# Optimization experiments

Measured on AMD Instinct MI355X. Metric: run time of the kernel, lower is better.

Reference implementation:

```python
import jax, jax.numpy as jnp
import numpy as np
from jax import lax

B, FREQ, TIME = 32, 256, 4096   # batch, freq bins, time frames
PAD_LEN = 256                   # cfg['n_peaks']
KSIZE = 5                       # cfg['blur_kernel']
SIGMA = 1.0                     # cfg['blur_sigma']


def setup_inputs() -> dict:
    key = jax.random.key(0)
    return {"spec_tensor": jax.random.normal(key, (B, FREQ, TIME), dtype=jnp.float32)}


def _peak_from_features(f):
    # local maxima along time (1x3) and freq (3x1), SAME padding, stride 1
    neg = jnp.asarray(-jnp.inf, f.dtype)
    max_t = lax.reduce_window(f, neg, lax.max, (1, 1, 3), (1, 1, 1), 'SAME')
    max_f = lax.reduce_window(f, neg, lax.max, (1, 3, 1), (1, 1, 1), 'SAME')
    peaks = ((f == max_t) & (f == max_f)).astype(f.dtype)
    mn = jnp.min(f, axis=(1, 2), keepdims=True)
    mx = jnp.max(f, axis=(1, 2), keepdims=True)
    return peaks * ((f - mn) / (mx - mn))


def _gaussian_blur(x):
    # separable gaussian blur with reflect padding (torchvision semantics)
    half = KSIZE // 2
    coords = jnp.arange(KSIZE, dtype=x.dtype) - half
    g = jnp.exp(-0.5 * (coords / SIGMA) ** 2)
    g = g / jnp.sum(g)
    x4 = jnp.pad(x, ((0, 0), (half, half), (half, half)), mode='reflect')[:, None]  # [B,1,F+2h,T+2h]
    kf = g.reshape(1, 1, KSIZE, 1)
    kt = g.reshape(1, 1, 1, KSIZE)
    y = lax.conv_general_dilated(x4, kf, (1, 1), 'VALID')
    y = lax.conv_general_dilated(y, kt, (1, 1), 'VALID')
    return y[:, 0]


def _extract(flat):
    # compact nonzero entries (row-major order) into fixed PAD_LEN slots, zero padded;
    # entries beyond PAD_LEN are truncated (scatter mode='drop').
    mask = flat > 0
    pos = jnp.cumsum(mask.astype(jnp.int32)) - 1
    dest = jnp.where(mask, pos, PAD_LEN)  # out-of-range -> dropped
    idx = jnp.zeros(PAD_LEN, jnp.int32).at[dest].set(
        jnp.arange(flat.shape[0], dtype=jnp.int32), mode='drop')
    val = jnp.zeros(PAD_LEN, flat.dtype).at[dest].set(flat, mode='drop')
    freq = (idx // TIME).astype(flat.dtype) / FREQ
    time = (idx % TIME).astype(flat.dtype) / TIME
    return jnp.stack([freq, time, val], axis=0)  # [3, PAD_LEN]


def reference(spec_tensor):
    p = _peak_from_features(spec_tensor)
    p = _gaussian_blur(p)
    p = _peak_from_features(p)
    return jax.vmap(_extract)(p.reshape(B, FREQ * TIME))  # [B, 3, PAD_LEN]
```

## Files before the change

kernel.cpp:

```cpp
#include <hip/hip_runtime.h>

#define NB 32
#define NF 256
#define NT 4096
#define PAD_LEN 256

#define TF 16
#define TT 128

#define TS 64
#define NSTRIP (NT / TS)

#define G0 0.054488684f
#define G1 0.24420134f
#define G2 0.40261995f

__device__ __forceinline__ float blur5(float a, float b, float c, float d, float e) {
    return G0 * (a + b) + G1 * (c + d) + G2 * e;
}
__device__ __forceinline__ float4 blur5v(const float4& a, const float4& b, const float4& c,
                                         const float4& d, const float4& e) {
    return make_float4(blur5(a.x, b.x, c.x, d.x, e.x), blur5(a.y, b.y, c.y, d.y, e.y),
                       blur5(a.z, b.z, c.z, d.z, e.z), blur5(a.w, b.w, c.w, d.w, e.w));
}

#define SW 140
#define SW4 35
#define RS 24
#define RP 22
#define RV 18

#define R1_WORDS (RS * SW)
#define R2_WORDS (RP * SW)

#define MPAD 20

__device__ __forceinline__ int reflectF(int i) {
    i = (i < 0) ? -i : i;
    return (i >= NF) ? (2 * NF - 2 - i) : i;
}
__device__ __forceinline__ unsigned encf(float x) {
    unsigned u = __float_as_uint(x);
    return (u & 0x80000000u) ? ~u : (u | 0x80000000u);
}
__device__ __forceinline__ float decf(unsigned e) {
    unsigned u = (e & 0x80000000u) ? (e ^ 0x80000000u) : ~e;
    return __uint_as_float(u);
}

#define MM_OFF 0
#define CNT_OFF 1024
#define PFX_OFF (1024 + NB * NF * 32 * 4)

__global__ __launch_bounds__(256) void k_init(float* __restrict__ out, unsigned* __restrict__ mm) {
    int tid = blockIdx.x * 256 + threadIdx.x;
    if (tid < NB * 3 * PAD_LEN) out[tid] = 0.0f;
    if (tid < NB) {
        mm[tid * 4 + 0] = 0xFFFFFFFFu;
        mm[tid * 4 + 1] = 0u;
        mm[tid * 4 + 2] = 0xFFFFFFFFu;
        mm[tid * 4 + 3] = 0u;
    }
}

__global__ __launch_bounds__(256) void k_minmax(const float* __restrict__ spec, unsigned* __restrict__ mm) {
    const int b = blockIdx.y;
    const float4* p = (const float4*)(spec + (size_t)b * NF * NT);
    const int base4 = blockIdx.x * 4096;
    float lmin = __builtin_inff(), lmax = -__builtin_inff();
    for (int i = threadIdx.x; i < 4096; i += 256) {
        float4 v = p[base4 + i];
        lmin = fminf(lmin, fminf(fminf(v.x, v.y), fminf(v.z, v.w)));
        lmax = fmaxf(lmax, fmaxf(fmaxf(v.x, v.y), fmaxf(v.z, v.w)));
    }
    for (int off = 32; off; off >>= 1) {
        lmin = fminf(lmin, __shfl_down(lmin, off));
        lmax = fmaxf(lmax, __shfl_down(lmax, off));
    }
    __shared__ float rmn[4], rmx[4];
    int wave = threadIdx.x >> 6, lane = threadIdx.x & 63;
    if (lane == 0) { rmn[wave] = lmin; rmx[wave] = lmax; }
    __syncthreads();
    if (threadIdx.x == 0) {
        for (int w = 1; w < 4; w++) { lmin = fminf(lmin, rmn[w]); lmax = fmaxf(lmax, rmx[w]); }
        atomicMin(&mm[b * 4 + 0], encf(lmin));
        atomicMax(&mm[b * 4 + 1], encf(lmax));
    }
}


template<int J> __device__ __forceinline__ float getj(const float4& v) {
    if constexpr (J == 0) return v.x;
    else if constexpr (J == 1) return v.y;
    else if constexpr (J == 2) return v.z;
    else return v.w;
}

template<bool DP, bool DH, bool DQ, int J>
__device__ __forceinline__ void march_step(
    const float4& r0, const float4& r1, const float4& r2, const float4& r3,
    float4& Sa, float4& Sb, float4& Sc,
    float4& V0, float4& V1, float4& V2, float4& V3, float4& V4,
    float4& Bm, float4& Bc, float4& Bp,
    int& c0, int& c1, int& c2, int& c3,
    float& lmin, float& lmax,
    const int lane, const int sid, const float mn, const float rinv, const int hb)
{
    const float NEGF = -__builtin_inff();
    float4 X = make_float4(getj<J>(r0), getj<J>(r1), getj<J>(r2), getj<J>(r3));
    Sa = Sb; Sb = Sc; Sc = X;
    if constexpr (DP) {
        float up0 = __shfl_up(Sb.w, 1);
        float dn3 = __shfl_down(Sb.x, 1);
        if (lane == 0)  up0 = NEGF;
        if (lane == 63) dn3 = NEGF;
        float4 P;
        { const float x = Sb.x; const bool pk = (x >= Sa.x) && (x >= Sc.x) && (x >= up0)  && (x >= Sb.y); P.x = pk ? (x - mn) * rinv : 0.0f; }
        { const float x = Sb.y; const bool pk = (x >= Sa.y) && (x >= Sc.y) && (x >= Sb.x) && (x >= Sb.z); P.y = pk ? (x - mn) * rinv : 0.0f; }
        { const float x = Sb.z; const bool pk = (x >= Sa.z) && (x >= Sc.z) && (x >= Sb.y) && (x >= Sb.w); P.z = pk ? (x - mn) * rinv : 0.0f; }
        { const float x = Sb.w; const bool pk = (x >= Sa.w) && (x >= Sc.w) && (x >= Sb.z) && (x >= dn3); P.w = pk ? (x - mn) * rinv : 0.0f; }
        const float pzm = __shfl_up(P.z, 1);
        const float pwm = __shfl_up(P.w, 1);
        const float pxp = __shfl_down(P.x, 1);
        const float pyp = __shfl_down(P.y, 1);
        float4 Vn;
        Vn.x = blur5(pzm, P.z, pwm, P.y, P.x);
        Vn.y = blur5(pwm, P.w, P.x, P.z, P.y);
        Vn.z = blur5(P.x, pxp, P.y, P.w, P.z);
        Vn.w = blur5(P.y, pyp, P.z, pxp, P.w);
        if (lane == 0)  { Vn.x = blur5(P.z, P.z, P.y, P.y, P.x);
                          Vn.y = blur5(P.y, P.w, P.x, P.z, P.y); }
        if (lane == 63) { Vn.z = blur5(P.x, P.z, P.y, P.w, P.z);
                          Vn.w = blur5(P.y, P.y, P.z, P.z, P.w); }
        V0 = V1; V1 = V2; V2 = V3; V3 = V4; V4 = Vn;
    }
    if constexpr (DH) {
        const int h = hb + J;
        float4 Bn;
        if ((unsigned)h < (unsigned)NT) {
            Bn = blur5v(V0, V4, V1, V3, V2);
            if (sid == 0) {
                if (h == 0)      Bn = blur5v(V4, V4, V3, V3, V2);
                else if (h == 1) Bn = blur5v(V2, V4, V1, V3, V2);
            }
            if (sid == NSTRIP - 1) {
                if (h == NT - 2)      Bn = blur5v(V0, V2, V1, V3, V2);
                else if (h == NT - 1) Bn = blur5v(V0, V0, V1, V1, V2);
            }
        } else {
            Bn = make_float4(NEGF, NEGF, NEGF, NEGF);
        }
        Bm = Bc; Bc = Bp; Bp = Bn;
    }
    if constexpr (DQ) {
        float u0 = __shfl_up(Bc.w, 1);
        float d3 = __shfl_down(Bc.x, 1);
        if (lane == 0)  u0 = NEGF;
        if (lane == 63) d3 = NEGF;
        { const float x = Bc.x; const bool pk = (x >= Bm.x) && (x >= Bp.x) && (x >= u0)   && (x >= Bc.y); c0 += (pk && (x > 0.0f)) ? 1 : 0; }
        { const float x = Bc.y; const bool pk = (x >= Bm.y) && (x >= Bp.y) && (x >= Bc.x) && (x >= Bc.z); c1 += (pk && (x > 0.0f)) ? 1 : 0; }
        { const float x = Bc.z; const bool pk = (x >= Bm.z) && (x >= Bp.z) && (x >= Bc.y) && (x >= Bc.w); c2 += (pk && (x > 0.0f)) ? 1 : 0; }
        { const float x = Bc.w; const bool pk = (x >= Bm.w) && (x >= Bp.w) && (x >= Bc.z) && (x >= d3); c3 += (pk && (x > 0.0f)) ? 1 : 0; }
        lmin = fminf(lmin, fminf(fminf(Bc.x, Bc.y), fminf(Bc.z, Bc.w)));
        lmax = fmaxf(lmax, fmaxf(fmaxf(Bc.x, Bc.y), fmaxf(Bc.z, Bc.w)));
    }
}

__global__ __launch_bounds__(256) void k_march(const float* __restrict__ spec,
                                               unsigned* __restrict__ mm,
                                               int* __restrict__ counts2) {
    const int b = blockIdx.y;
    const int lane = threadIdx.x & 63;
    const int wv = threadIdx.x >> 6;
    const int sid = blockIdx.x * 4 + wv;
    const int T0 = sid * TS;

    const float mn = decf(mm[b * 4 + 0]);
    const float mx = decf(mm[b * 4 + 1]);
    const float rinv = 1.0f / (mx - mn);

    const float NEGF = -__builtin_inff();
    const float4 NEG4 = make_float4(NEGF, NEGF, NEGF, NEGF);

    __shared__ __align__(16) float sStage[4][256 * MPAD];
    float* myS = sStage[wv];

    const int lrow = lane >> 2;
    const int lq = lane & 3;
    const float* gb = spec + (size_t)b * NF * NT;

    float4 R[16];
    float4 A[4];

#define GLOAD(J) do {                                                           \
    const int tg = T0 - 16 + 16 * (J);                                          \
    if ((unsigned)tg < (unsigned)NT) {                                          \
        const float* gp = gb + (size_t)lrow * NT + tg + 4 * lq;                 \
        _Pragma("unroll")                                                       \
        for (int i = 0; i < 16; ++i)                                            \
            R[i] = *(const float4*)(gp + (size_t)(16 * i) * NT);                \
    } else {                                                                    \
        _Pragma("unroll")                                                       \
        for (int i = 0; i < 16; ++i) R[i] = NEG4;                               \
    }                                                                           \
} while (0)

#define SWRITE() do {                                                           \
    _Pragma("unroll")                                                           \
    for (int i = 0; i < 16; ++i) {                                              \
        const int row_ = 16 * i + lrow;                                         \
        const int q_ = (row_ * 5 + lq) ^ ((row_ >> 2) & 7);                     \
        *(float4*)(myS + 4 * q_) = R[i];                                        \
    }                                                                           \
} while (0)

#define SREAD(C) do {                                                           \
    _Pragma("unroll")                                                           \
    for (int j = 0; j < 4; ++j) {                                               \
        const int row_ = 4 * lane + j;                                          \
        const int q_ = (row_ * 5 + ((C) >> 2)) ^ (lane & 7);                    \
        A[j] = *(const float4*)(myS + 4 * q_);                                  \
    }                                                                           \
} while (0)

    float4 Sa = NEG4, Sb = NEG4, Sc = NEG4;
    float4 V0 = NEG4, V1 = NEG4, V2 = NEG4, V3 = NEG4, V4 = NEG4;
    float4 Bm = NEG4, Bc = NEG4, Bp = NEG4;
    int c0 = 0, c1 = 0, c2 = 0, c3 = 0;
    float lmin = __builtin_inff(), lmax = NEGF;

#define MARGS Sa, Sb, Sc, V0, V1, V2, V3, V4, Bm, Bc, Bp, c0, c1, c2, c3, lmin, lmax, lane, sid, mn, rinv

#define SET_FULL(C, HB) do { SREAD(C); const int hb_ = (HB);                    \
    march_step<true, true, true, 0>(A[0], A[1], A[2], A[3], MARGS, hb_);        \
    march_step<true, true, true, 1>(A[0], A[1], A[2], A[3], MARGS, hb_);        \
    march_step<true, true, true, 2>(A[0], A[1], A[2], A[3], MARGS, hb_);        \
    march_step<true, true, true, 3>(A[0], A[1], A[2], A[3], MARGS, hb_); } while (0)

    GLOAD(0);
    SWRITE();
    GLOAD(1);
    SREAD(12);
    march_step<false, false, false, 0>(A[0], A[1], A[2], A[3], MARGS, 0);
    march_step<false, false, false, 1>(A[0], A[1], A[2], A[3], MARGS, 0);
    march_step<true,  false, false, 2>(A[0], A[1], A[2], A[3], MARGS, 0);
    march_step<true,  false, false, 3>(A[0], A[1], A[2], A[3], MARGS, 0);
    SWRITE();
    GLOAD(2);
    {
        const int hb_ = T0 - 3;
        SREAD(0);
        march_step<true, false, false, 0>(A[0], A[1], A[2], A[3], MARGS, hb_);
        march_step<true, false, false, 1>(A[0], A[1], A[2], A[3], MARGS, hb_);
        march_step<true, true,  false, 2>(A[0], A[1], A[2], A[3], MARGS, hb_);
        march_step<true, true,  false, 3>(A[0], A[1], A[2], A[3], MARGS, hb_);
    }
    SET_FULL(4,  T0 + 1);
    SET_FULL(8,  T0 + 5);
    SET_FULL(12, T0 + 9);
    SWRITE(); GLOAD(3);
    SET_FULL(0,  T0 + 13); SET_FULL(4,  T0 + 17); SET_FULL(8,  T0 + 21); SET_FULL(12, T0 + 25);
    SWRITE(); GLOAD(4);
    SET_FULL(0,  T0 + 29); SET_FULL(4,  T0 + 33); SET_FULL(8,  T0 + 37); SET_FULL(12, T0 + 41);
    SWRITE(); GLOAD(5);
    SET_FULL(0,  T0 + 45); SET_FULL(4,  T0 + 49); SET_FULL(8,  T0 + 53); SET_FULL(12, T0 + 57);
    SWRITE();
    SET_FULL(0,  T0 + 61);

#undef SET_FULL
#undef GLOAD
#undef SWRITE
#undef SREAD
#undef MARGS

    int* sc = (int*)&sStage[0][0];
    __syncthreads();
    sc[threadIdx.x * 4 + 0] = c0;
    sc[threadIdx.x * 4 + 1] = c1;
    sc[threadIdx.x * 4 + 2] = c2;
    sc[threadIdx.x * 4 + 3] = c3;
    __syncthreads();
    if ((wv & 1) == 0) {
        const int p = (threadIdx.x + 64) * 4;
        const int cc = sid >> 1;
        const int fr = 4 * lane;
        counts2[(b * NF + fr + 0) * 32 + cc] = c0 + sc[p + 0];
        counts2[(b * NF + fr + 1) * 32 + cc] = c1 + sc[p + 1];
        counts2[(b * NF + fr + 2) * 32 + cc] = c2 + sc[p + 2];
        counts2[(b * NF + fr + 3) * 32 + cc] = c3 + sc[p + 3];
    }

    for (int off = 32; off; off >>= 1) {
        lmin = fminf(lmin, __shfl_down(lmin, off));
        lmax = fmaxf(lmax, __shfl_down(lmax, off));
    }
    if (lane == 0) {
        atomicMin(&mm[b * 4 + 2], encf(lmin));
        atomicMax(&mm[b * 4 + 3], encf(lmax));
    }
}

__device__ __forceinline__ void blur_tile(const float* __restrict__ sb_base,
                                          int f0, int t0, float mn, float rinv,
                                          float* sR1, float* sR2, int tid,
                                          bool f_lo, bool f_hi, bool t_lo, bool t_hi) {
    const float NEG = -__builtin_inff();
    float* sS = sR1;
    float* sV = sR1;
    float* sB = sR2;
    float4* sS4 = (float4*)sR1;
    float4* sP4 = (float4*)sR2;
    float4* sV4 = (float4*)sR1;
    float4* sB4 = (float4*)sR2;

    const bool f_edge = f_lo || f_hi;
    const bool t_edge = t_lo || t_hi;
    const int lane = tid & 63;

    if (!f_edge && !t_edge) {
        const float4* gp = (const float4*)(sb_base + (size_t)(f0 - 4) * NT + (t0 - 4));
        for (int i = tid; i < RS * 34; i += 256) {
            int r = i / 34, c = i - r * 34;
            sS4[r * SW4 + c] = gp[r * (NT / 4) + c];
        }
    } else {
        for (int i = tid; i < RS * 34; i += 256) {
            int r = i / 34, c = i - r * 34;
            int gf = f0 - 4 + r;
            int gc0 = t0 - 4 + 4 * c;
            float4 v = make_float4(NEG, NEG, NEG, NEG);
            if ((unsigned)gf < NF && (unsigned)gc0 < NT)
                v = *(const float4*)(sb_base + (size_t)gf * NT + gc0);
            sS4[r * SW4 + c] = v;
        }
    }
    __syncthreads();

    for (int i = tid; i < RP * 34; i += 256) {
        int r = i / 34, g = i - r * 34;
        const float4 c4 = sS4[(r + 1) * SW4 + g];
        const float4 u4 = sS4[r * SW4 + g];
        const float4 d4 = sS4[(r + 2) * SW4 + g];
        float lm = __shfl_up(c4.w, 1);
        float rp = __shfl_down(c4.x, 1);
        if (lane == 0 && g > 0)   lm = sS[(r + 1) * SW + 4 * g - 1];
        if (lane == 63 && g < 33) rp = sS[(r + 1) * SW + 4 * g + 4];
        float4 o;
        o.x = (c4.x >= lm   && c4.x >= c4.y && c4.x >= u4.x && c4.x >= d4.x) ? (c4.x - mn) * rinv : 0.0f;
        o.y = (c4.y >= c4.x && c4.y >= c4.z && c4.y >= u4.y && c4.y >= d4.y) ? (c4.y - mn) * rinv : 0.0f;
        o.z = (c4.z >= c4.y && c4.z >= c4.w && c4.z >= u4.z && c4.z >= d4.z) ? (c4.z - mn) * rinv : 0.0f;
        o.w = (c4.w >= c4.z && c4.w >= rp   && c4.w >= u4.w && c4.w >= d4.w) ? (c4.w - mn) * rinv : 0.0f;
        if (g == 0) o.x = 0.0f;
        if (g == 33) o.w = 0.0f;
        sP4[r * SW4 + g] = o;
    }
    __syncthreads();

    if (!f_edge) {
        for (int i = tid; i < RV * 34; i += 256) {
            int r = i / 34, g = i - r * 34;
            const float4 p0 = sP4[r * SW4 + g];
            const float4 p1 = sP4[(r + 1) * SW4 + g];
            const float4 p2 = sP4[(r + 2) * SW4 + g];
            const float4 p3 = sP4[(r + 3) * SW4 + g];
            const float4 p4 = sP4[(r + 4) * SW4 + g];
            sV4[r * SW4 + g] = blur5v(p0, p4, p1, p3, p2);
        }
    } else {
        for (int i = tid; i < RV * 34; i += 256) {
            int r = i / 34, g = i - r * 34;
            const int gf = f0 - 1 + r;
            const int r0 = reflectF(gf - 2) - (f0 - 3);
            const int r1 = reflectF(gf - 1) - (f0 - 3);
            const int r2 = gf - (f0 - 3);
            const int r3 = reflectF(gf + 1) - (f0 - 3);
            const int r4 = reflectF(gf + 2) - (f0 - 3);
            const float4 p0 = sP4[r0 * SW4 + g];
            const float4 p1 = sP4[r1 * SW4 + g];
            const float4 p2 = sP4[r2 * SW4 + g];
            const float4 p3 = sP4[r3 * SW4 + g];
            const float4 p4 = sP4[r4 * SW4 + g];
            sV4[r * SW4 + g] = blur5v(p0, p4, p1, p3, p2);
        }
    }
    __syncthreads();

    for (int i = tid; i < RV * 32; i += 256) {
        int r = i >> 5, g = 1 + (i & 31);
        const float4 A = sV4[r * SW4 + g - 1];
        const float4 B = sV4[r * SW4 + g];
        const float4 C = sV4[r * SW4 + g + 1];
        float4 o;
        o.x = blur5(A.z, B.z, A.w, B.y, B.x);
        o.y = blur5(A.w, B.w, B.x, B.z, B.y);
        o.z = blur5(B.x, C.x, B.y, B.w, B.z);
        o.w = blur5(B.y, C.y, B.z, C.x, B.w);
        if (t_lo && g == 1) {
            o.x = blur5(B.z, B.z, B.y, B.y, B.x);
            o.y = blur5(B.y, B.w, B.x, B.z, B.y);
        }
        if (t_hi && g == 32) {
            o.z = blur5(B.x, B.z, B.y, B.w, B.z);
            o.w = blur5(B.y, B.y, B.z, B.z, B.w);
        }
        if ((f_lo && r == 0) || (f_hi && r == 17)) o = make_float4(NEG, NEG, NEG, NEG);
        sB4[r * SW4 + g] = o;
    }
    for (int i = tid; i < RV * 2; i += 256) {
        int r = i >> 1;
        int hi = i & 1;
        int s = hi ? 132 : 3;
        const float* vr = sV + r * SW;
        float v = blur5(vr[s - 2], vr[s + 2], vr[s - 1], vr[s + 1], vr[s]);
        if ((hi ? t_hi : t_lo) || (f_lo && r == 0) || (f_hi && r == 17)) v = NEG;
        sB[r * SW + s] = v;
    }
    __syncthreads();
}

struct Win8 {
    float c[8], l[8], rr[8], u[8], d[8];
};
__device__ __forceinline__ void load_win8(const float4* sB4, int r, int m, Win8& w) {
    const int g = 1 + 2 * m;
    const float4 Cm = sB4[(r + 1) * SW4 + g - 1];
    const float4 C0 = sB4[(r + 1) * SW4 + g];
    const float4 C1 = sB4[(r + 1) * SW4 + g + 1];
    const float4 C2 = sB4[(r + 1) * SW4 + g + 2];
    const float4 U0 = sB4[r * SW4 + g];
    const float4 U1 = sB4[r * SW4 + g + 1];
    const float4 D0 = sB4[(r + 2) * SW4 + g];
    const float4 D1 = sB4[(r + 2) * SW4 + g + 1];
    w.c[0] = C0.x; w.c[1] = C0.y; w.c[2] = C0.z; w.c[3] = C0.w;
    w.c[4] = C1.x; w.c[5] = C1.y; w.c[6] = C1.z; w.c[7] = C1.w;
    w.l[0] = Cm.w; w.l[1] = C0.x; w.l[2] = C0.y; w.l[3] = C0.z;
    w.l[4] = C0.w; w.l[5] = C1.x; w.l[6] = C1.y; w.l[7] = C1.z;
    w.rr[0] = C0.y; w.rr[1] = C0.z; w.rr[2] = C0.w; w.rr[3] = C1.x;
    w.rr[4] = C1.y; w.rr[5] = C1.z; w.rr[6] = C1.w; w.rr[7] = C2.x;
    w.u[0] = U0.x; w.u[1] = U0.y; w.u[2] = U0.z; w.u[3] = U0.w;
    w.u[4] = U1.x; w.u[5] = U1.y; w.u[6] = U1.z; w.u[7] = U1.w;
    w.d[0] = D0.x; w.d[1] = D0.y; w.d[2] = D0.z; w.d[3] = D0.w;
    w.d[4] = D1.x; w.d[5] = D1.y; w.d[6] = D1.z; w.d[7] = D1.w;
}

__global__ __launch_bounds__(256) void k_prefix(const float* __restrict__ spec,
                                                unsigned* __restrict__ mm,
                                                int* __restrict__ counts2,
                                                int* __restrict__ prefix2) {
    const int b = blockIdx.x;
    const int tid = threadIdx.x;
    const float mn2 = decf(mm[b * 4 + 2]);
    if (mn2 != 0.0f) {
        __shared__ __align__(16) float sR1[R1_WORDS];
        __shared__ __align__(16) float sR2[R2_WORDS];
        const float4* sB4 = (const float4*)sR2;
        const float mn = decf(mm[b * 4 + 0]);
        const float mx = decf(mm[b * 4 + 1]);
        const float rinv = 1.0f / (mx - mn);
        const float* sb_base = spec + (size_t)b * NF * NT;
        int* pcnt = (int*)sR1;
        for (int ty = 0; ty < NF / TF; ++ty)
        for (int tx = 0; tx < NT / TT; ++tx) {
            blur_tile(sb_base, ty * TF, tx * TT, mn, rinv, sR1, sR2, tid,
                      ty == 0, ty == NF / TF - 1, tx == 0, tx == NT / TT - 1);
            const int r = tid & 15, m = tid >> 4;
            Win8 w;
            load_win8(sB4, r, m, w);
            int cnt = 0;
#pragma unroll
            for (int k = 0; k < 8; k++) {
                float x = w.c[k];
                bool pk = (x >= w.l[k]) && (x >= w.rr[k]) && (x >= w.u[k]) && (x >= w.d[k]);
                cnt += (pk && (x > mn2)) ? 1 : 0;
            }
            (void)m;
            const int lane = tid & 63, wvv = tid >> 6;
            int cs = cnt;
            cs += __shfl_down(cs, 32);
            cs += __shfl_down(cs, 16);
            if (lane < 16) pcnt[wvv * 16 + lane] = cs;
            __syncthreads();
            if (tid < 16)
                counts2[(b * NF + ty * TF + tid) * 32 + tx] =
                    pcnt[tid] + pcnt[16 + tid] + pcnt[32 + tid] + pcnt[48 + tid];
            __syncthreads();
        }
    }
    const int* cb = counts2 + b * NF * 32;
    int* pb = prefix2 + b * NF * 32;
    int local[32];
    int s = 0;
    for (int c = 0; c < 32; c++) {
        local[c] = cb[tid * 32 + c];
        s += local[c];
    }
    __shared__ int tot[256];
    tot[tid] = s;
    __syncthreads();
    for (int off = 1; off < 256; off <<= 1) {
        int v = (tid >= off) ? tot[tid - off] : 0;
        __syncthreads();
        tot[tid] += v;
        __syncthreads();
    }
    int run = tot[tid] - s;
    for (int c = 0; c < 32; c++) {
        pb[tid * 32 + c] = run;
        run += local[c];
    }
}

__global__ __launch_bounds__(256) void k_extract(const float* __restrict__ spec, unsigned* __restrict__ mm,
                                                 const int* __restrict__ prefix2, float* __restrict__ out) {
    const int b = blockIdx.z;
    const int f0 = blockIdx.y * TF;
    const int t0 = blockIdx.x * TT;
    const int c0 = blockIdx.x;
    if (prefix2[(b * NF + f0) * 32 + c0] >= PAD_LEN) return;

    const int tid = threadIdx.x;
    __shared__ __align__(16) float sR1[R1_WORDS];
    __shared__ __align__(16) float sR2[R2_WORDS];
    const float4* sB4 = (const float4*)sR2;

    const float mn = decf(mm[b * 4 + 0]);
    const float mx = decf(mm[b * 4 + 1]);
    const float rinv = 1.0f / (mx - mn);
    const float mn2 = decf(mm[b * 4 + 2]);
    const float mx2 = decf(mm[b * 4 + 3]);
    const float rinv2 = 1.0f / (mx2 - mn2);
    const float* sb_base = spec + (size_t)b * NF * NT;

    const bool f_lo = (blockIdx.y == 0), f_hi = (blockIdx.y == NF / TF - 1);
    const bool t_lo = (blockIdx.x == 0), t_hi = (blockIdx.x == NT / TT - 1);
    blur_tile(sb_base, f0, t0, mn, rinv, sR1, sR2, tid, f_lo, f_hi, t_lo, t_hi);

    const int r = tid & 15, m = tid >> 4;
    const int gf = f0 + r;
    const int base = prefix2[(b * NF + gf) * 32 + c0];
    Win8 w;
    load_win8(sB4, r, m, w);
    bool pos[8];
    int mycnt = 0;
#pragma unroll
    for (int k = 0; k < 8; k++) {
        float x = w.c[k];
        pos[k] = (x >= w.l[k]) && (x >= w.rr[k]) && (x >= w.u[k]) && (x >= w.d[k]) && (x > mn2);
        mycnt += pos[k] ? 1 : 0;
    }
    const int lane = tid & 63, wv = tid >> 6, p = (tid >> 4) & 3;
    int s = mycnt;
    int t1 = __shfl_up(s, 16); if (p >= 1) s += t1;
    int t2 = __shfl_up(s, 32); if (p >= 2) s += t2;
    __shared__ int wtot[4][16];
    if (p == 3) wtot[wv][lane & 15] = s;
    __syncthreads();
    int woff = 0;
    for (int w2 = 0; w2 < wv; ++w2) woff += wtot[w2][r];
    int rank = base + woff + (s - mycnt);
#pragma unroll
    for (int k = 0; k < 8; k++) {
        if (pos[k]) {
            if (rank < PAD_LEN) {
                int gc = t0 + 8 * m + k;
                out[b * 768 + rank]       = (float)gf * (1.0f / 256.0f);
                out[b * 768 + 256 + rank] = (float)gc * (1.0f / 4096.0f);
                out[b * 768 + 512 + rank] = (w.c[k] - mn2) * rinv2;
            }
            rank++;
        }
    }
}

extern "C" void kernel_launch(void* const* d_in, const int* in_sizes, int n_in,
                              void* d_out, int out_size, void* d_ws, size_t ws_size,
                              hipStream_t stream) {
    const float* spec = (const float*)d_in[0];
    float* out = (float*)d_out;
    unsigned* mm = (unsigned*)((char*)d_ws + MM_OFF);
    int* counts2 = (int*)((char*)d_ws + CNT_OFF);
    int* prefix2 = (int*)((char*)d_ws + PFX_OFF);

    k_init<<<96, 256, 0, stream>>>(out, mm);
    k_minmax<<<dim3(64, NB), 256, 0, stream>>>(spec, mm);
    k_march<<<dim3(NSTRIP / 4, NB), 256, 0, stream>>>(spec, mm, counts2);
    k_prefix<<<NB, 256, 0, stream>>>(spec, mm, counts2, prefix2);
    dim3 tgrid(NT / TT, NF / TF, NB);
    k_extract<<<tgrid, 256, 0, stream>>>(spec, mm, prefix2, out);
}
```

Baseline: 330.7 us.

## Fuse prefix and extract into one per-batch tail kernel; shrink march smem padding

Merges the prefix-scan kernel and the tiled extract kernel into a single per-batch kernel. It walks tiles in row-major order, skips tiles with zero peaks and stops once the running prefix reaches PAD_LEN. This removes one launch and the large grid of extract blocks, most of which exit early or do redundant blur work. In exchange, extraction runs serially over tiles within one block per batch, which is only 32 blocks. Separately, the march shared-memory stride drops from 5 to 4 float4 per row (MPAD 20→16), and the read swizzle now uses the row-based XOR so it matches the write side.

```diff
diff --git a/kernel.cpp b/kernel.cpp
--- a/kernel.cpp
+++ b/kernel.cpp
@@ -33,7 +33,7 @@
 #define R1_WORDS (RS * SW)
 #define R2_WORDS (RP * SW)
 
-#define MPAD 20
+#define MPAD 16
 
 __device__ __forceinline__ int reflectF(int i) {
     i = (i < 0) ? -i : i;
@@ -209,7 +209,7 @@
     _Pragma("unroll")                                                           \
     for (int i = 0; i < 16; ++i) {                                              \
         const int row_ = 16 * i + lrow;                                         \
-        const int q_ = (row_ * 5 + lq) ^ ((row_ >> 2) & 7);                     \
+        const int q_ = (row_ * 4 + lq) ^ ((row_ >> 2) & 7);                     \
         *(float4*)(myS + 4 * q_) = R[i];                                        \
     }                                                                           \
 } while (0)
@@ -218,7 +218,7 @@
     _Pragma("unroll")                                                           \
     for (int j = 0; j < 4; ++j) {                                               \
         const int row_ = 4 * lane + j;                                          \
-        const int q_ = (row_ * 5 + ((C) >> 2)) ^ (lane & 7);                    \
+        const int q_ = (row_ * 4 + ((C) >> 2)) ^ ((row_ >> 2) & 7);             \
         A[j] = *(const float4*)(myS + 4 * q_);                                  \
     }                                                                           \
 } while (0)
@@ -443,21 +443,26 @@
     w.d[4] = D1.x; w.d[5] = D1.y; w.d[6] = D1.z; w.d[7] = D1.w;
 }
 
-__global__ __launch_bounds__(256) void k_prefix(const float* __restrict__ spec,
-                                                unsigned* __restrict__ mm,
-                                                int* __restrict__ counts2,
-                                                int* __restrict__ prefix2) {
+__global__ __launch_bounds__(256) void k_tail(const float* __restrict__ spec,
+                                              unsigned* __restrict__ mm,
+                                              int* __restrict__ counts2,
+                                              int* __restrict__ prefix2,
+                                              float* __restrict__ out) {
     const int b = blockIdx.x;
     const int tid = threadIdx.x;
+    __shared__ __align__(16) float sR1[R1_WORDS];
+    __shared__ __align__(16) float sR2[R2_WORDS];
+    const float4* sB4 = (const float4*)sR2;
+
+    const float mn = decf(mm[b * 4 + 0]);
+    const float mx = decf(mm[b * 4 + 1]);
+    const float rinv = 1.0f / (mx - mn);
     const float mn2 = decf(mm[b * 4 + 2]);
+    const float mx2 = decf(mm[b * 4 + 3]);
+    const float rinv2 = 1.0f / (mx2 - mn2);
+    const float* sb_base = spec + (size_t)b * NF * NT;
+
     if (mn2 != 0.0f) {
-        __shared__ __align__(16) float sR1[R1_WORDS];
-        __shared__ __align__(16) float sR2[R2_WORDS];
-        const float4* sB4 = (const float4*)sR2;
-        const float mn = decf(mm[b * 4 + 0]);
-        const float mx = decf(mm[b * 4 + 1]);
-        const float rinv = 1.0f / (mx - mn);
-        const float* sb_base = spec + (size_t)b * NF * NT;
         int* pcnt = (int*)sR1;
         for (int ty = 0; ty < NF / TF; ++ty)
         for (int tx = 0; tx < NT / TT; ++tx) {
@@ -486,88 +491,87 @@
             __syncthreads();
         }
     }
+
     const int* cb = counts2 + b * NF * 32;
     int* pb = prefix2 + b * NF * 32;
-    int local[32];
-    int s = 0;
-    for (int c = 0; c < 32; c++) {
-        local[c] = cb[tid * 32 + c];
-        s += local[c];
-    }
-    __shared__ int tot[256];
-    tot[tid] = s;
-    __syncthreads();
-    for (int off = 1; off < 256; off <<= 1) {
-        int v = (tid >= off) ? tot[tid - off] : 0;
+    {
+        int local[32];
+        int s = 0;
+        for (int c = 0; c < 32; c++) {
+            local[c] = cb[tid * 32 + c];
+            s += local[c];
+        }
+        __shared__ int tot[256];
+        tot[tid] = s;
         __syncthreads();
-        tot[tid] += v;
+        for (int off = 1; off < 256; off <<= 1) {
+            int v = (tid >= off) ? tot[tid - off] : 0;
+            __syncthreads();
+            tot[tid] += v;
+            __syncthreads();
+        }
+        int run = tot[tid] - s;
+        for (int c = 0; c < 32; c++) {
+            pb[tid * 32 + c] = run;
+            run += local[c];
+        }
+    }
+
+    __shared__ int sInfo[2];
+    __shared__ int wtot[4][16];
+    for (int t = 0; t < (NF / TF) * (NT / TT); ++t) {
+        const int ty = t >> 5, tx = t & 31;
+        const int f0 = ty * TF, t0 = tx * TT;
         __syncthreads();
-    }
-    int run = tot[tid] - s;
-    for (int c = 0; c < 32; c++) {
-        pb[tid * 32 + c] = run;
-        run += local[c];
-    }
-}
-
-__global__ __launch_bounds__(256) void k_extract(const float* __restrict__ spec, unsigned* __restrict__ mm,
-                                                 const int* __restrict__ prefix2, float* __restrict__ out) {
-    const int b = blockIdx.z;
-    const int f0 = blockIdx.y * TF;
-    const int t0 = blockIdx.x * TT;
-    const int c0 = blockIdx.x;
-    if (prefix2[(b * NF + f0) * 32 + c0] >= PAD_LEN) return;
-
-    const int tid = threadIdx.x;
-    __shared__ __align__(16) float sR1[R1_WORDS];
-    __shared__ __align__(16) float sR2[R2_WORDS];
-    const float4* sB4 = (const float4*)sR2;
-
-    const float mn = decf(mm[b * 4 + 0]);
-    const float mx = decf(mm[b * 4 + 1]);
-    const float rinv = 1.0f / (mx - mn);
-    const float mn2 = decf(mm[b * 4 + 2]);
-    const float mx2 = decf(mm[b * 4 + 3]);
-    const float rinv2 = 1.0f / (mx2 - mn2);
-    const float* sb_base = spec + (size_t)b * NF * NT;
-
-    const bool f_lo = (blockIdx.y == 0), f_hi = (blockIdx.y == NF / TF - 1);
-    const bool t_lo = (blockIdx.x == 0), t_hi = (blockIdx.x == NT / TT - 1);
-    blur_tile(sb_base, f0, t0, mn, rinv, sR1, sR2, tid, f_lo, f_hi, t_lo, t_hi);
-
-    const int r = tid & 15, m = tid >> 4;
-    const int gf = f0 + r;
-    const int base = prefix2[(b * NF + gf) * 32 + c0];
-    Win8 w;
-    load_win8(sB4, r, m, w);
-    bool pos[8];
-    int mycnt = 0;
+        if (tid == 0) sInfo[0] = pb[f0 * 32 + tx];
+        int tc = 0;
+        if (tid < 16) tc = cb[(f0 + tid) * 32 + tx];
+        tc += __shfl_down(tc, 8, 16);
+        tc += __shfl_down(tc, 4, 16);
+        tc += __shfl_down(tc, 2, 16);
+        tc += __shfl_down(tc, 1, 16);
+        if (tid == 0) sInfo[1] = tc;
+        __syncthreads();
+        if (sInfo[0] >= PAD_LEN) break;
+        if (sInfo[1] == 0) continue;
+
+        const bool f_lo = (ty == 0), f_hi = (ty == NF / TF - 1);
+        const bool t_lo = (tx == 0), t_hi = (tx == NT / TT - 1);
+        blur_tile(sb_base, f0, t0, mn, rinv, sR1, sR2, tid, f_lo, f_hi, t_lo, t_hi);
+
+        const int r = tid & 15, m = tid >> 4;
+        const int gf = f0 + r;
+        const int base = pb[gf * 32 + tx];
+        Win8 w;
+        load_win8(sB4, r, m, w);
+        bool pos[8];
+        int mycnt = 0;
 #pragma unroll
-    for (int k = 0; k < 8; k++) {
-        float x = w.c[k];
-        pos[k] = (x >= w.l[k]) && (x >= w.rr[k]) && (x >= w.u[k]) && (x >= w.d[k]) && (x > mn2);
-        mycnt += pos[k] ? 1 : 0;
-    }
-    const int lane = tid & 63, wv = tid >> 6, p = (tid >> 4) & 3;
-    int s = mycnt;
-    int t1 = __shfl_up(s, 16); if (p >= 1) s += t1;
-    int t2 = __shfl_up(s, 32); if (p >= 2) s += t2;
-    __shared__ int wtot[4][16];
-    if (p == 3) wtot[wv][lane & 15] = s;
-    __syncthreads();
-    int woff = 0;
-    for (int w2 = 0; w2 < wv; ++w2) woff += wtot[w2][r];
-    int rank = base + woff + (s - mycnt);
+        for (int k = 0; k < 8; k++) {
+            float x = w.c[k];
+            pos[k] = (x >= w.l[k]) && (x >= w.rr[k]) && (x >= w.u[k]) && (x >= w.d[k]) && (x > mn2);
+            mycnt += pos[k] ? 1 : 0;
+        }
+        const int lane = tid & 63, wv = tid >> 6, p = (tid >> 4) & 3;
+        int s = mycnt;
+        int t1 = __shfl_up(s, 16); if (p >= 1) s += t1;
+        int t2 = __shfl_up(s, 32); if (p >= 2) s += t2;
+        if (p == 3) wtot[wv][lane & 15] = s;
+        __syncthreads();
+        int woff = 0;
+        for (int w2 = 0; w2 < wv; ++w2) woff += wtot[w2][r];
+        int rank = base + woff + (s - mycnt);
 #pragma unroll
-    for (int k = 0; k < 8; k++) {
-        if (pos[k]) {
-            if (rank < PAD_LEN) {
-                int gc = t0 + 8 * m + k;
-                out[b * 768 + rank]       = (float)gf * (1.0f / 256.0f);
-                out[b * 768 + 256 + rank] = (float)gc * (1.0f / 4096.0f);
-                out[b * 768 + 512 + rank] = (w.c[k] - mn2) * rinv2;
+        for (int k = 0; k < 8; k++) {
+            if (pos[k]) {
+                if (rank < PAD_LEN) {
+                    int gc = t0 + 8 * m + k;
+                    out[b * 768 + rank]       = (float)gf * (1.0f / 256.0f);
+                    out[b * 768 + 256 + rank] = (float)gc * (1.0f / 4096.0f);
+                    out[b * 768 + 512 + rank] = (w.c[k] - mn2) * rinv2;
+                }
+                rank++;
             }
-            rank++;
         }
     }
 }
@@ -584,7 +588,5 @@
     k_init<<<96, 256, 0, stream>>>(out, mm);
     k_minmax<<<dim3(64, NB), 256, 0, stream>>>(spec, mm);
     k_march<<<dim3(NSTRIP / 4, NB), 256, 0, stream>>>(spec, mm, counts2);
-    k_prefix<<<NB, 256, 0, stream>>>(spec, mm, counts2, prefix2);
-    dim3 tgrid(NT / TT, NF / TF, NB);
-    k_extract<<<tgrid, 256, 0, stream>>>(spec, mm, prefix2, out);
-}
+    k_tail<<<NB, 256, 0, stream>>>(spec, mm, counts2, prefix2, out);
+}
```

Result: slower. 392.5 us (+18.7%).

## Halve march strip width to 32 frames and raise k_march occupancy

Applied to the files above, without the earlier changes.

Reduces the time strip handled per wavefront from 64 to 32 frames, so each load stage stages 8 float4 rows instead of 16. This shrinks register and LDS footprint and adds a launch bound of 3 blocks per SM. It also changes the LDS swizzle layout, clamps edge loads in place of the conditional -inf fill (with explicit masking at the first and last strips), and sums the per-wave counts across all 4 waves in a block. The cost is a larger halo-to-work ratio, since the 3-frame halo is now recomputed over fewer frames, and twice as many blocks.

```diff
diff --git a/kernel.cpp b/kernel.cpp
--- a/kernel.cpp
+++ b/kernel.cpp
@@ -8,7 +8,7 @@
 #define TF 16
 #define TT 128
 
-#define TS 64
+#define TS 32
 #define NSTRIP (NT / TS)
 
 #define G0 0.054488684f
@@ -32,8 +32,6 @@
 
 #define R1_WORDS (RS * SW)
 #define R2_WORDS (RP * SW)
-
-#define MPAD 20
 
 __device__ __forceinline__ int reflectF(int i) {
     i = (i < 0) ? -i : i;
@@ -166,9 +164,9 @@
     }
 }
 
-__global__ __launch_bounds__(256) void k_march(const float* __restrict__ spec,
-                                               unsigned* __restrict__ mm,
-                                               int* __restrict__ counts2) {
+__global__ __launch_bounds__(256, 3) void k_march(const float* __restrict__ spec,
+                                                  unsigned* __restrict__ mm,
+                                                  int* __restrict__ counts2) {
     const int b = blockIdx.y;
     const int lane = threadIdx.x & 63;
     const int wv = threadIdx.x >> 6;
@@ -182,45 +180,35 @@
     const float NEGF = -__builtin_inff();
     const float4 NEG4 = make_float4(NEGF, NEGF, NEGF, NEGF);
 
-    __shared__ __align__(16) float sStage[4][256 * MPAD];
-    float* myS = sStage[wv];
-
-    const int lrow = lane >> 2;
-    const int lq = lane & 3;
+    __shared__ __align__(16) float sBuf[4][2048];
+    float4* myS4 = (float4*)sBuf[wv];
+
+    const int srow = lane >> 1;
+    const int sq = lane & 1;
     const float* gb = spec + (size_t)b * NF * NT;
 
-    float4 R[16];
+    float4 R[8];
     float4 A[4];
 
-#define GLOAD(J) do {                                                           \
-    const int tg = T0 - 16 + 16 * (J);                                          \
-    if ((unsigned)tg < (unsigned)NT) {                                          \
-        const float* gp = gb + (size_t)lrow * NT + tg + 4 * lq;                 \
-        _Pragma("unroll")                                                       \
-        for (int i = 0; i < 16; ++i)                                            \
-            R[i] = *(const float4*)(gp + (size_t)(16 * i) * NT);                \
-    } else {                                                                    \
-        _Pragma("unroll")                                                       \
-        for (int i = 0; i < 16; ++i) R[i] = NEG4;                               \
-    }                                                                           \
+#define GLOAD(G) do {                                                           \
+    int tg_ = T0 - 8 + 8 * (G) + 4 * sq;                                        \
+    tg_ = (tg_ < 0) ? 0 : ((tg_ > NT - 4) ? (NT - 4) : tg_);                    \
+    const float* gp_ = gb + (size_t)srow * NT + tg_;                            \
+    _Pragma("unroll")                                                           \
+    for (int i = 0; i < 8; ++i)                                                 \
+        R[i] = *(const float4*)(gp_ + (size_t)(32 * i) * NT);                   \
 } while (0)
 
-#define SWRITE() do {                                                           \
+#define WRITE() do {                                                            \
     _Pragma("unroll")                                                           \
-    for (int i = 0; i < 16; ++i) {                                              \
-        const int row_ = 16 * i + lrow;                                         \
-        const int q_ = (row_ * 5 + lq) ^ ((row_ >> 2) & 7);                     \
-        *(float4*)(myS + 4 * q_) = R[i];                                        \
-    }                                                                           \
+    for (int i = 0; i < 8; ++i)                                                 \
+        myS4[(64 * i + lane) ^ ((lane >> 3) & 7)] = R[i];                       \
 } while (0)
 
-#define SREAD(C) do {                                                           \
+#define SREAD(QC) do {                                                          \
     _Pragma("unroll")                                                           \
-    for (int j = 0; j < 4; ++j) {                                               \
-        const int row_ = 4 * lane + j;                                          \
-        const int q_ = (row_ * 5 + ((C) >> 2)) ^ (lane & 7);                    \
-        A[j] = *(const float4*)(myS + 4 * q_);                                  \
-    }                                                                           \
+    for (int j = 0; j < 4; ++j)                                                 \
+        A[j] = myS4[(8 * lane + 2 * j + (QC)) ^ (lane & 7)];                    \
 } while (0)
 
     float4 Sa = NEG4, Sb = NEG4, Sc = NEG4;
@@ -231,22 +219,22 @@
 
 #define MARGS Sa, Sb, Sc, V0, V1, V2, V3, V4, Bm, Bc, Bp, c0, c1, c2, c3, lmin, lmax, lane, sid, mn, rinv
 
-#define SET_FULL(C, HB) do { SREAD(C); const int hb_ = (HB);                    \
+#define SET_FULL(HB) do { const int hb_ = (HB);                                 \
     march_step<true, true, true, 0>(A[0], A[1], A[2], A[3], MARGS, hb_);        \
     march_step<true, true, true, 1>(A[0], A[1], A[2], A[3], MARGS, hb_);        \
     march_step<true, true, true, 2>(A[0], A[1], A[2], A[3], MARGS, hb_);        \
     march_step<true, true, true, 3>(A[0], A[1], A[2], A[3], MARGS, hb_); } while (0)
 
-    GLOAD(0);
-    SWRITE();
-    GLOAD(1);
-    SREAD(12);
+    GLOAD(0); WRITE(); GLOAD(1);
+
+    SREAD(1);
+    if (sid == 0) { A[0] = NEG4; A[1] = NEG4; A[2] = NEG4; A[3] = NEG4; }
     march_step<false, false, false, 0>(A[0], A[1], A[2], A[3], MARGS, 0);
     march_step<false, false, false, 1>(A[0], A[1], A[2], A[3], MARGS, 0);
     march_step<true,  false, false, 2>(A[0], A[1], A[2], A[3], MARGS, 0);
     march_step<true,  false, false, 3>(A[0], A[1], A[2], A[3], MARGS, 0);
-    SWRITE();
-    GLOAD(2);
+
+    WRITE(); GLOAD(2);
     {
         const int hb_ = T0 - 3;
         SREAD(0);
@@ -255,39 +243,44 @@
         march_step<true, true,  false, 2>(A[0], A[1], A[2], A[3], MARGS, hb_);
         march_step<true, true,  false, 3>(A[0], A[1], A[2], A[3], MARGS, hb_);
     }
-    SET_FULL(4,  T0 + 1);
-    SET_FULL(8,  T0 + 5);
-    SET_FULL(12, T0 + 9);
-    SWRITE(); GLOAD(3);
-    SET_FULL(0,  T0 + 13); SET_FULL(4,  T0 + 17); SET_FULL(8,  T0 + 21); SET_FULL(12, T0 + 25);
-    SWRITE(); GLOAD(4);
-    SET_FULL(0,  T0 + 29); SET_FULL(4,  T0 + 33); SET_FULL(8,  T0 + 37); SET_FULL(12, T0 + 41);
-    SWRITE(); GLOAD(5);
-    SET_FULL(0,  T0 + 45); SET_FULL(4,  T0 + 49); SET_FULL(8,  T0 + 53); SET_FULL(12, T0 + 57);
-    SWRITE();
-    SET_FULL(0,  T0 + 61);
+    SREAD(1); SET_FULL(T0 + 1);
+
+    WRITE(); GLOAD(3);
+    SREAD(0); SET_FULL(T0 + 5);
+    SREAD(1); SET_FULL(T0 + 9);
+
+    WRITE(); GLOAD(4);
+    SREAD(0); SET_FULL(T0 + 13);
+    SREAD(1); SET_FULL(T0 + 17);
+
+    WRITE(); GLOAD(5);
+    SREAD(0); SET_FULL(T0 + 21);
+    SREAD(1); SET_FULL(T0 + 25);
+
+    WRITE();
+    SREAD(0);
+    if (sid == NSTRIP - 1) { A[0] = NEG4; A[1] = NEG4; A[2] = NEG4; A[3] = NEG4; }
+    SET_FULL(T0 + 29);
 
 #undef SET_FULL
 #undef GLOAD
-#undef SWRITE
+#undef WRITE
 #undef SREAD
 #undef MARGS
 
-    int* sc = (int*)&sStage[0][0];
-    __syncthreads();
+    __syncthreads();
+    int* sc = (int*)&sBuf[0][0];
     sc[threadIdx.x * 4 + 0] = c0;
     sc[threadIdx.x * 4 + 1] = c1;
     sc[threadIdx.x * 4 + 2] = c2;
     sc[threadIdx.x * 4 + 3] = c3;
     __syncthreads();
-    if ((wv & 1) == 0) {
-        const int p = (threadIdx.x + 64) * 4;
-        const int cc = sid >> 1;
-        const int fr = 4 * lane;
-        counts2[(b * NF + fr + 0) * 32 + cc] = c0 + sc[p + 0];
-        counts2[(b * NF + fr + 1) * 32 + cc] = c1 + sc[p + 1];
-        counts2[(b * NF + fr + 2) * 32 + cc] = c2 + sc[p + 2];
-        counts2[(b * NF + fr + 3) * 32 + cc] = c3 + sc[p + 3];
+    {
+        const int r = threadIdx.x;
+        const int l = r >> 2, j = r & 3;
+        int tot = sc[(0 * 64 + l) * 4 + j] + sc[(1 * 64 + l) * 4 + j]
+                + sc[(2 * 64 + l) * 4 + j] + sc[(3 * 64 + l) * 4 + j];
+        counts2[(b * NF + r) * 32 + blockIdx.x] = tot;
     }
 
     for (int off = 32; off; off >>= 1) {
```

Result: slower. 362.7 us (+9.7%).
